# Performance work log

Measured on AMD Instinct MI355X. Metric: run time of the kernel, lower is better.

## Reference

```python
import jax, jax.numpy as jnp
import numpy as np

N = 8192
IN_F = 512
OUT_F = 64
ALPHA = 0.2  # LeakyReLU negative slope
NEG_INF = -9e15


def setup_inputs() -> dict:
    key = jax.random.key(0)
    k1, k2, k3, k4 = jax.random.split(key, 4)
    x = jax.random.normal(k1, (N, IN_F), dtype=jnp.float32)
    adj = jax.random.randint(k2, (N, N), 0, 2, dtype=jnp.int32)
    # xavier_uniform with gain=1.414
    def xavier(k, shape, gain=1.414):
        fan_in, fan_out = shape[0], shape[1]
        a = gain * np.sqrt(6.0 / (fan_in + fan_out))
        return jax.random.uniform(k, shape, jnp.float32, -a, a)
    W = xavier(k3, (IN_F, OUT_F))
    a = xavier(k4, (2 * OUT_F, 1))
    return {"x": x, "adj": adj, "W": W, "a": a}


def reference(x, adj, W, a):
    h = x @ W  # [N, F]
    f = W.shape[1]
    # e[i,j] = leakyrelu([h_i, h_j] @ a) = leakyrelu(h_i@a1 + h_j@a2)
    e1 = h @ a[:f, 0]   # [N]
    e2 = h @ a[f:, 0]   # [N]
    e = jax.nn.leaky_relu(e1[:, None] + e2[None, :], negative_slope=ALPHA)  # [N, N]
    scores = jnp.where(adj > 0, e, NEG_INF)
    attention = jax.nn.softmax(scores, axis=1)  # dropout p=0.0 -> identity
    h_prime = attention @ h  # [N, F]
    return jax.nn.elu(h_prime)  # concat=True
```

## Files before the change

kernel.cpp:

```cpp
#include <hip/hip_runtime.h>
#include <hip/hip_bf16.h>

#define NN 8192
#define KF 512
#define FF 64
#define GAT_ALPHA 0.2f
#define MSHIFT 20.0f
#define LOG2E 1.44269504f

#define JSPLIT 16
#define JW (NN / JSPLIT)
#define KSTEPS (JW / 32)

#define EXP2F(x) __builtin_amdgcn_exp2f(x)

typedef __attribute__((ext_vector_type(8))) __bf16 bf16x8;
typedef __attribute__((ext_vector_type(4))) float f32x4;

__global__ __launch_bounds__(256) void gat_linear(
    const float* __restrict__ x, const float* __restrict__ W,
    const float* __restrict__ av, __hip_bfloat16* __restrict__ ht,
    float* __restrict__ e1, float* __restrict__ e2)
{
    __shared__ float xs[32][33];
    __shared__ float Ws[32][64];
    __shared__ float ep[2][32][17];

    const int t  = threadIdx.x;
    const int fq = t & 15;
    const int rq = t >> 4;
    const int i0 = blockIdx.x * 32;

    const int kl = t & 31, r0 = t >> 5;
    const int fw = t & 63, kq = t >> 6;

    float acc[2][4] = {};

    for (int kt = 0; kt < KF; kt += 32) {
        #pragma unroll
        for (int m = 0; m < 4; ++m)
            xs[kl][r0 + 8 * m] = x[(size_t)(i0 + r0 + 8 * m) * KF + kt + kl];
        #pragma unroll
        for (int m = 0; m < 8; ++m)
            Ws[kq + 4 * m][fw] = W[(size_t)(kt + kq + 4 * m) * FF + fw];
        __syncthreads();
        #pragma unroll
        for (int kk = 0; kk < 32; ++kk) {
            float x0 = xs[kk][rq * 2];
            float x1 = xs[kk][rq * 2 + 1];
            f32x4 wv = *(const f32x4*)&Ws[kk][fq * 4];
            #pragma unroll
            for (int v = 0; v < 4; ++v) {
                acc[0][v] += x0 * wv[v];
                acc[1][v] += x1 * wv[v];
            }
        }
        __syncthreads();
    }

    #pragma unroll
    for (int v = 0; v < 4; ++v) {
        int f = fq * 4 + v;
        union { ushort2 q; __hip_bfloat16 h[2]; } pk;
        pk.h[0] = __float2bfloat16(acc[0][v]);
        pk.h[1] = __float2bfloat16(acc[1][v]);
        *(ushort2*)&ht[(size_t)f * NN + i0 + rq * 2] = pk.q;
    }

    f32x4 a1v = *(const f32x4*)&av[fq * 4];
    f32x4 a2v = *(const f32x4*)&av[64 + fq * 4];
    #pragma unroll
    for (int u = 0; u < 2; ++u) {
        float s1 = 0.f, s2 = 0.f;
        #pragma unroll
        for (int v = 0; v < 4; ++v) {
            s1 += acc[u][v] * a1v[v];
            s2 += acc[u][v] * a2v[v];
        }
        ep[0][rq * 2 + u][fq] = s1;
        ep[1][rq * 2 + u][fq] = s2;
    }
    __syncthreads();
    if (t < 32) {
        float s1 = 0.f, s2 = 0.f;
        #pragma unroll
        for (int q = 0; q < 16; ++q) { s1 += ep[0][t][q]; s2 += ep[1][t][q]; }
        e1[i0 + t] = s1 * LOG2E;
        e2[i0 + t] = s2 * LOG2E;
    }
}

__global__ __launch_bounds__(256, 4) void gat_attn(
    const int* __restrict__ adj, const __hip_bfloat16* __restrict__ ht,
    const float* __restrict__ e1, const float* __restrict__ e2,
    float* __restrict__ accs, float* __restrict__ lsums)
{
    const int t     = threadIdx.x;
    const int lane  = t & 63;
    const int wv    = t >> 6;
    const int n16   = lane & 15;
    const int quad  = lane >> 4;
    const int split = blockIdx.x & (JSPLIT - 1);
    const int i0    = (blockIdx.x >> 4) * 64 + wv * 16;
    const int j0    = split * JW;
    const int row   = i0 + n16;

    const float e1L = e1[row];
    float ms = e1L + MSHIFT * LOG2E;
    const float miL = ms > 0.f ? ms : GAT_ALPHA * ms;

    const int*            ap  = adj + (size_t)row * NN + j0 + quad * 8;
    const float*          epx = e2 + j0 + quad * 8;
    const __hip_bfloat16* hp  = ht + (size_t)n16 * NN + j0 + quad * 8;

    int4   aA[2][2];
    float4 eA[2][2];
    bf16x8 bA[2][4];
    float lpart = 0.f;
    f32x4 dacc[4] = {{0.f,0.f,0.f,0.f},{0.f,0.f,0.f,0.f},{0.f,0.f,0.f,0.f},{0.f,0.f,0.f,0.f}};

#define LOADB(sl, st)                                                         \
    {                                                                         \
        aA[sl][0] = *(const int4*)(ap + (st) * 32);                           \
        aA[sl][1] = *(const int4*)(ap + (st) * 32 + 4);                       \
        eA[sl][0] = *(const float4*)(epx + (st) * 32);                        \
        eA[sl][1] = *(const float4*)(epx + (st) * 32 + 4);                    \
        bA[sl][0] = *(const bf16x8*)(hp + (size_t)(st) * 32);                 \
        bA[sl][1] = *(const bf16x8*)(hp + (size_t)16 * NN + (st) * 32);       \
        bA[sl][2] = *(const bf16x8*)(hp + (size_t)32 * NN + (st) * 32);       \
        bA[sl][3] = *(const bf16x8*)(hp + (size_t)48 * NN + (st) * 32);       \
    }

    LOADB(0, 0)
    LOADB(1, 1)

    #pragma unroll
    for (int st = 0; st < KSTEPS; ++st) {
        const int sl = st & 1;
        union { bf16x8 v; __hip_bfloat16 h[8]; } af;
        const int*   av4 = (const int*)&aA[sl][0];
        const float* ev4 = (const float*)&eA[sl][0];
        #pragma unroll
        for (int jj = 0; jj < 8; ++jj) {
            float s_ = e1L + ev4[jj];
            s_ = s_ > 0.f ? s_ : GAT_ALPHA * s_;
            float p_ = av4[jj] > 0 ? EXP2F(s_ - miL) : 0.f;
            af.h[jj] = __float2bfloat16(p_);
            lpart += __bfloat162float(af.h[jj]);
        }
        bf16x8 b0 = bA[sl][0], b1 = bA[sl][1], b2 = bA[sl][2], b3 = bA[sl][3];
        if (st + 2 < KSTEPS) LOADB(sl, st + 2)
        dacc[0] = __builtin_amdgcn_mfma_f32_16x16x32_bf16(af.v, b0, dacc[0], 0, 0, 0);
        dacc[1] = __builtin_amdgcn_mfma_f32_16x16x32_bf16(af.v, b1, dacc[1], 0, 0, 0);
        dacc[2] = __builtin_amdgcn_mfma_f32_16x16x32_bf16(af.v, b2, dacc[2], 0, 0, 0);
        dacc[3] = __builtin_amdgcn_mfma_f32_16x16x32_bf16(af.v, b3, dacc[3], 0, 0, 0);
    }
#undef LOADB

    lpart += __shfl_xor(lpart, 16);
    lpart += __shfl_xor(lpart, 32);
    if (quad == 0) lsums[(size_t)split * NN + row] = lpart;

    float* ab = accs + (size_t)split * NN * FF;
    #pragma unroll
    for (int ft = 0; ft < 4; ++ft)
        #pragma unroll
        for (int r = 0; r < 4; ++r)
            ab[(size_t)(i0 + quad * 4 + r) * FF + ft * 16 + n16] = dacc[ft][r];
}

__global__ __launch_bounds__(256) void gat_epilogue(
    const float* __restrict__ accs, const float* __restrict__ lsums,
    float* __restrict__ out)
{
    const int idx = (blockIdx.x * 256 + threadIdx.x) * 4;
    const int row = idx >> 6;

    float l = 0.f;
    #pragma unroll
    for (int s = 0; s < JSPLIT; ++s) l += lsums[(size_t)s * NN + row];

    f32x4 a = {0.f, 0.f, 0.f, 0.f};
    #pragma unroll
    for (int s = 0; s < JSPLIT; ++s) {
        f32x4 v = *(const f32x4*)(accs + (size_t)s * NN * FF + idx);
        a.x += v.x; a.y += v.y; a.z += v.z; a.w += v.w;
    }

    const float li = 1.f / l;
    f32x4 o;
    #pragma unroll
    for (int v = 0; v < 4; ++v) {
        float hv = a[v] * li;
        o[v] = hv > 0.f ? hv : __expf(hv) - 1.f;
    }
    *(f32x4*)(out + idx) = o;
}

extern "C" void kernel_launch(void* const* d_in, const int* in_sizes, int n_in,
                              void* d_out, int out_size, void* d_ws, size_t ws_size,
                              hipStream_t stream) {
    const float* x   = (const float*)d_in[0];
    const int*   adj = (const int*)d_in[1];
    const float* W   = (const float*)d_in[2];
    const float* av  = (const float*)d_in[3];
    float* out = (float*)d_out;

    char* wsb = (char*)d_ws;
    __hip_bfloat16* ht = (__hip_bfloat16*)wsb;
    float* e1    = (float*)(wsb + (1 << 20));
    float* e2    = e1 + NN;
    float* accs  = e2 + NN;
    float* lsums = accs + (size_t)JSPLIT * NN * FF;

    gat_linear<<<256, 256, 0, stream>>>(x, W, av, ht, e1, e2);
    gat_attn<<<(NN / 64) * JSPLIT, 256, 0, stream>>>(adj, ht, e1, e2, accs, lsums);
    gat_epilogue<<<NN * FF / 1024, 256, 0, stream>>>(accs, lsums, out);
}
```

Before: 427.5 us.

## Compute row sums via MFMA with ones, deepen adj prefetch, simplify leaky-exp

The row-sum accumulation of the bf16 probabilities moves off the VALU and onto an extra MFMA that multiplies the probability tile by a ones vector. The cross-lane shuffle reduction goes away, and each lane now writes a row sum taken straight from the MFMA output. LeakyReLU plus the shift is rewritten as the max of two precomputed affine terms, so each element needs one add, one fma, one max and one exp2. Adjacency loads become nontemporal and are prefetched three steps ahead instead of two, which adds register pressure under the 4-wave occupancy bound.

```diff
diff --git a/kernel.cpp b/kernel.cpp
--- a/kernel.cpp
+++ b/kernel.cpp
@@ -16,6 +16,7 @@
 
 typedef __attribute__((ext_vector_type(8))) __bf16 bf16x8;
 typedef __attribute__((ext_vector_type(4))) float f32x4;
+typedef __attribute__((ext_vector_type(4))) int   i32x4;
 
 __global__ __launch_bounds__(256) void gat_linear(
     const float* __restrict__ x, const float* __restrict__ W,
@@ -108,58 +109,82 @@
     const float e1L = e1[row];
     float ms = e1L + MSHIFT * LOG2E;
     const float miL = ms > 0.f ? ms : GAT_ALPHA * ms;
+    const float c0  = e1L - miL;
+    const float c1  = GAT_ALPHA * e1L - miL;
 
     const int*            ap  = adj + (size_t)row * NN + j0 + quad * 8;
     const float*          epx = e2 + j0 + quad * 8;
     const __hip_bfloat16* hp  = ht + (size_t)n16 * NN + j0 + quad * 8;
 
-    int4   aA[2][2];
+    i32x4  aA[3][2];
     float4 eA[2][2];
     bf16x8 bA[2][4];
-    float lpart = 0.f;
     f32x4 dacc[4] = {{0.f,0.f,0.f,0.f},{0.f,0.f,0.f,0.f},{0.f,0.f,0.f,0.f},{0.f,0.f,0.f,0.f}};
-
-#define LOADB(sl, st)                                                         \
-    {                                                                         \
-        aA[sl][0] = *(const int4*)(ap + (st) * 32);                           \
-        aA[sl][1] = *(const int4*)(ap + (st) * 32 + 4);                       \
-        eA[sl][0] = *(const float4*)(epx + (st) * 32);                        \
-        eA[sl][1] = *(const float4*)(epx + (st) * 32 + 4);                    \
-        bA[sl][0] = *(const bf16x8*)(hp + (size_t)(st) * 32);                 \
-        bA[sl][1] = *(const bf16x8*)(hp + (size_t)16 * NN + (st) * 32);       \
-        bA[sl][2] = *(const bf16x8*)(hp + (size_t)32 * NN + (st) * 32);       \
-        bA[sl][3] = *(const bf16x8*)(hp + (size_t)48 * NN + (st) * 32);       \
-    }
-
-    LOADB(0, 0)
-    LOADB(1, 1)
+    f32x4 dl = {0.f, 0.f, 0.f, 0.f};
+
+    union { unsigned short s[8]; bf16x8 v; } ones;
+    #pragma unroll
+    for (int k = 0; k < 8; ++k) ones.s[k] = 0x3F80;
+
+#define LOADA(sl, st)                                                          \
+    {                                                                          \
+        aA[sl][0] = __builtin_nontemporal_load((const i32x4*)(ap + (st) * 32));\
+        aA[sl][1] = __builtin_nontemporal_load((const i32x4*)(ap + (st) * 32 + 4));\
+    }
+#define LOADE(sl, st)                                                          \
+    {                                                                          \
+        eA[sl][0] = *(const float4*)(epx + (st) * 32);                         \
+        eA[sl][1] = *(const float4*)(epx + (st) * 32 + 4);                     \
+    }
+#define LOADH(sl, st)                                                          \
+    {                                                                          \
+        bA[sl][0] = *(const bf16x8*)(hp + (size_t)(st) * 32);                  \
+        bA[sl][1] = *(const bf16x8*)(hp + (size_t)16 * NN + (st) * 32);        \
+        bA[sl][2] = *(const bf16x8*)(hp + (size_t)32 * NN + (st) * 32);        \
+        bA[sl][3] = *(const bf16x8*)(hp + (size_t)48 * NN + (st) * 32);        \
+    }
+
+    LOADA(0, 0) LOADA(1, 1) LOADA(2, 2)
+    LOADE(0, 0) LOADE(1, 1)
+    LOADH(0, 0) LOADH(1, 1)
 
     #pragma unroll
     for (int st = 0; st < KSTEPS; ++st) {
-        const int sl = st & 1;
+        const int s3 = st % 3, s2 = st & 1;
+        i32x4  a0 = aA[s3][0], a1 = aA[s3][1];
+        float4 e0 = eA[s2][0], ev = eA[s2][1];
+        bf16x8 b0 = bA[s2][0], b1 = bA[s2][1], b2 = bA[s2][2], b3 = bA[s2][3];
+
+        if (st + 3 < KSTEPS) LOADA(s3, st + 3)
+        if (st + 2 < KSTEPS) { LOADE(s2, st + 2) LOADH(s2, st + 2) }
+
         union { bf16x8 v; __hip_bfloat16 h[8]; } af;
-        const int*   av4 = (const int*)&aA[sl][0];
-        const float* ev4 = (const float*)&eA[sl][0];
-        #pragma unroll
-        for (int jj = 0; jj < 8; ++jj) {
-            float s_ = e1L + ev4[jj];
-            s_ = s_ > 0.f ? s_ : GAT_ALPHA * s_;
-            float p_ = av4[jj] > 0 ? EXP2F(s_ - miL) : 0.f;
-            af.h[jj] = __float2bfloat16(p_);
-            lpart += __bfloat162float(af.h[jj]);
+#define PJ(idx, aval, eval)                                                    \
+        {                                                                      \
+            float t0 = c0 + (eval);                                            \
+            float t1 = __builtin_fmaf(GAT_ALPHA, (eval), c1);                  \
+            float p_ = EXP2F(fmaxf(t0, t1));                                   \
+            af.h[idx] = __float2bfloat16((aval) > 0 ? p_ : 0.f);               \
         }
-        bf16x8 b0 = bA[sl][0], b1 = bA[sl][1], b2 = bA[sl][2], b3 = bA[sl][3];
-        if (st + 2 < KSTEPS) LOADB(sl, st + 2)
+        PJ(0, a0.x, e0.x) PJ(1, a0.y, e0.y) PJ(2, a0.z, e0.z) PJ(3, a0.w, e0.w)
+        PJ(4, a1.x, ev.x) PJ(5, a1.y, ev.y) PJ(6, a1.z, ev.z) PJ(7, a1.w, ev.w)
+#undef PJ
+
         dacc[0] = __builtin_amdgcn_mfma_f32_16x16x32_bf16(af.v, b0, dacc[0], 0, 0, 0);
         dacc[1] = __builtin_amdgcn_mfma_f32_16x16x32_bf16(af.v, b1, dacc[1], 0, 0, 0);
         dacc[2] = __builtin_amdgcn_mfma_f32_16x16x32_bf16(af.v, b2, dacc[2], 0, 0, 0);
         dacc[3] = __builtin_amdgcn_mfma_f32_16x16x32_bf16(af.v, b3, dacc[3], 0, 0, 0);
-    }
-#undef LOADB
-
-    lpart += __shfl_xor(lpart, 16);
-    lpart += __shfl_xor(lpart, 32);
-    if (quad == 0) lsums[(size_t)split * NN + row] = lpart;
+        dl      = __builtin_amdgcn_mfma_f32_16x16x32_bf16(af.v, ones.v, dl, 0, 0, 0);
+    }
+#undef LOADA
+#undef LOADE
+#undef LOADH
+
+    if (n16 == 0) {
+        #pragma unroll
+        for (int r = 0; r < 4; ++r)
+            lsums[(size_t)split * NN + i0 + quad * 4 + r] = dl[r];
+    }
 
     float* ab = accs + (size_t)split * NN * FF;
     #pragma unroll
```

Result: slower. 448.5 us (+4.9%).
